# Kernel tuning notes

Measured on AMD Instinct MI355X. Metric: run time of the kernel, lower is better.

The kernel has to match this reference:

```python
import jax, jax.numpy as jnp
import numpy as np

SIGMA = 0.1
EPS = 1e-12

def setup_inputs() -> dict:
    key = jax.random.key(0)
    emb_org = jax.random.normal(key, (8192, 256), dtype=jnp.float32)
    return {"emb_org": emb_org}

def reference(emb_org):
    # L2-normalize rows (clamp norm at 1e-12 like torch)
    norm = jnp.clip(jnp.linalg.norm(emb_org, axis=1, keepdims=True), EPS, None)
    emb_n = emb_org / norm                      # [N, D]
    W = jnp.matmul(emb_n, emb_n.T) / SIGMA      # [N, N] cosine sim / sigma
    T = jax.nn.softmax(W, axis=1)               # row softmax
    emb_sft = jnp.matmul(T, emb_org)            # [N, D]
    return emb_sft
```

## Files before the change

kernel.cpp:

```cpp
#include <hip/hip_runtime.h>
#include <hip/hip_bf16.h>
#include <stdint.h>

#define NROWS 8192
#define DDIM  256
#define SIGMA_INV 10.0f

#define BM 64
#define BN 64
#define NSPLIT 4
#define JCHUNK (NROWS / NSPLIT)
#define NITER  (JCHUNK / BN)
#define PSTR   72
#define KCHB   1056

typedef __attribute__((ext_vector_type(8))) short bf16x8;
typedef __attribute__((ext_vector_type(4))) float f32x4;

__device__ inline unsigned short f2bf(float x) {
  __hip_bfloat16 h = __float2bfloat16(x);
  return *reinterpret_cast<unsigned short*>(&h);
}

__device__ inline void dma16(const void* g, void* l) {
  __builtin_amdgcn_global_load_lds(
      (const __attribute__((address_space(1))) unsigned int*)g,
      (__attribute__((address_space(3))) unsigned int*)l, 16, 0, 0);
}

__global__ __launch_bounds__(256) void normalize_k(const float* __restrict__ emb,
                                                   unsigned short* __restrict__ embn) {
  const int w = threadIdx.x >> 6, lane = threadIdx.x & 63;
  const int row = blockIdx.x * 4 + w;
  const float4* src = (const float4*)(emb + (size_t)row * DDIM);
  float4 v = src[lane];
  float ss = v.x * v.x + v.y * v.y + v.z * v.z + v.w * v.w;
  for (int off = 32; off >= 1; off >>= 1) ss += __shfl_xor(ss, off);
  const float sc = 1.0f / fmaxf(sqrtf(ss), 1e-12f);
  ushort4 o;
  o.x = f2bf(v.x * sc); o.y = f2bf(v.y * sc);
  o.z = f2bf(v.z * sc); o.w = f2bf(v.w * sc);
  ((ushort4*)(embn + (size_t)row * DDIM))[lane] = o;
}

__global__ __launch_bounds__(256) void transpose_k(const float* __restrict__ emb,
                                                   unsigned short* __restrict__ vt) {
  __shared__ float tile[64][65];
  const int r0 = blockIdx.x * 64, c0 = blockIdx.y * 64;
  const int tr = threadIdx.x >> 6, tc = threadIdx.x & 63;
  for (int i = 0; i < 16; ++i)
    tile[i * 4 + tr][tc] = emb[(size_t)(r0 + i * 4 + tr) * DDIM + c0 + tc];
  __syncthreads();
  for (int i = 0; i < 16; ++i)
    vt[(size_t)(c0 + i * 4 + tr) * NROWS + r0 + tc] = f2bf(tile[tc][i * 4 + tr]);
}

__global__ __launch_bounds__(256, 2) void fused_k(
    const unsigned short* __restrict__ embn,
    const unsigned short* __restrict__ vt,
    float* __restrict__ out,
    float* __restrict__ l_part)
{
  __shared__ char kn[32 * KCHB];
  __shared__ unsigned short pl[BM * PSTR];

  const int tid = threadIdx.x;
  const int w = tid >> 6, lane = tid & 63;
  const int mg = w >> 1, dh = w & 1;
  const int q = lane >> 4, c = lane & 15;
  const int chunk = blockIdx.x & 3;
  const int mblk = blockIdx.x >> 2;
  const int row0 = mblk * BM + mg * 32;
  const size_t j0base = (size_t)chunk * JCHUNK;

  bf16x8 qa[2][8];
  for (int mt = 0; mt < 2; ++mt)
    for (int k = 0; k < 8; ++k)
      qa[mt][k] = *(const bf16x8*)(embn + (size_t)(row0 + mt * 16 + c) * DDIM + k * 32 + q * 8);

  f32x4 oacc[2][8];
  for (int mt = 0; mt < 2; ++mt)
    for (int u = 0; u < 8; ++u) oacc[mt][u] = {0.f, 0.f, 0.f, 0.f};
  float lacc[2][4] = {};

  {
    const char* src = (const char*)(embn + j0base * DDIM);
    for (int cc = 0; cc < 8; ++cc) {
      const int ch = w * 8 + cc;
      dma16(src + ch * 1024 + lane * 16, kn + ch * KCHB + lane * 16);
    }
  }

  for (int it = 0; it < NITER; ++it) {
    const size_t j0 = j0base + (size_t)it * BN;
    __syncthreads();

    f32x4 sacc[2][2];
    for (int mt = 0; mt < 2; ++mt)
      for (int nt = 0; nt < 2; ++nt) sacc[mt][nt] = {0.f, 0.f, 0.f, 0.f};
    const int rb0 = (dh * 16 + (c >> 1)) * KCHB + (c & 1) * 512;
    const int rb1 = (dh * 16 + 8 + (c >> 1)) * KCHB + (c & 1) * 512;
    for (int k = 0; k < 8; ++k) {
      bf16x8 b0 = *(const bf16x8*)(kn + rb0 + k * 64 + q * 16);
      bf16x8 b1 = *(const bf16x8*)(kn + rb1 + k * 64 + q * 16);
      for (int mt = 0; mt < 2; ++mt) {
        sacc[mt][0] = __builtin_amdgcn_mfma_f32_16x16x32_bf16(qa[mt][k], b0, sacc[mt][0], 0, 0, 0);
        sacc[mt][1] = __builtin_amdgcn_mfma_f32_16x16x32_bf16(qa[mt][k], b1, sacc[mt][1], 0, 0, 0);
      }
    }

    bf16x8 vfrag[2][8];
    for (int kk = 0; kk < 2; ++kk)
      for (int u = 0; u < 8; ++u) {
        const int d = dh * 128 + u * 16 + c;
        vfrag[kk][u] = *(const bf16x8*)(vt + (size_t)d * NROWS + j0 + kk * 32 + q * 8);
      }

    for (int mt = 0; mt < 2; ++mt)
      for (int nt = 0; nt < 2; ++nt)
        for (int r = 0; r < 4; ++r) {
          const float p = __expf(fmaf(SIGMA_INV, sacc[mt][nt][r], -SIGMA_INV));
          lacc[mt][r] += p;
          pl[(mg * 32 + mt * 16 + q * 4 + r) * PSTR + dh * 32 + nt * 16 + c] = f2bf(p);
        }

    __syncthreads();

    for (int kk = 0; kk < 2; ++kk) {
      bf16x8 ap0 = *(const bf16x8*)(pl + (mg * 32 + c) * PSTR + kk * 32 + q * 8);
      bf16x8 ap1 = *(const bf16x8*)(pl + (mg * 32 + 16 + c) * PSTR + kk * 32 + q * 8);
      for (int u = 0; u < 8; ++u) {
        oacc[0][u] = __builtin_amdgcn_mfma_f32_16x16x32_bf16(ap0, vfrag[kk][u], oacc[0][u], 0, 0, 0);
        oacc[1][u] = __builtin_amdgcn_mfma_f32_16x16x32_bf16(ap1, vfrag[kk][u], oacc[1][u], 0, 0, 0);
      }
    }

    if (it + 1 < NITER) {
      const char* src = (const char*)(embn + (j0base + (size_t)(it + 1) * BN) * DDIM);
      for (int cc = 0; cc < 8; ++cc) {
        const int ch = w * 8 + cc;
        dma16(src + ch * 1024 + lane * 16, kn + ch * KCHB + lane * 16);
      }
    }
  }

  for (int mt = 0; mt < 2; ++mt)
    for (int r = 0; r < 4; ++r) {
      float s = lacc[mt][r];
      s += __shfl_xor(s, 1); s += __shfl_xor(s, 2);
      s += __shfl_xor(s, 4); s += __shfl_xor(s, 8);
      if (c == 0)
        atomicAdd(&l_part[row0 + mt * 16 + q * 4 + r], s);
    }
  for (int mt = 0; mt < 2; ++mt)
    for (int u = 0; u < 8; ++u)
      for (int r = 0; r < 4; ++r)
        atomicAdd(&out[(size_t)(row0 + mt * 16 + q * 4 + r) * DDIM + dh * 128 + u * 16 + c],
                  oacc[mt][u][r]);
}

__global__ __launch_bounds__(256) void finalize_k(float* __restrict__ out,
                                                  const float* __restrict__ l_part) {
  const int row = blockIdx.x, t = threadIdx.x;
  out[(size_t)row * DDIM + t] /= l_part[row];
}

extern "C" void kernel_launch(void* const* d_in, const int* in_sizes, int n_in,
                              void* d_out, int out_size, void* d_ws, size_t ws_size,
                              hipStream_t stream) {
  const float* emb = (const float*)d_in[0];
  float* out = (float*)d_out;
  char* ws = (char*)d_ws;
  unsigned short* embn = (unsigned short*)ws;
  unsigned short* vt   = (unsigned short*)(ws + ((size_t)4 << 20));
  float* l_part        = (float*)(ws + ((size_t)8 << 20));

  hipMemsetAsync(out, 0, (size_t)NROWS * DDIM * sizeof(float), stream);
  hipMemsetAsync(l_part, 0, (size_t)NROWS * sizeof(float), stream);

  normalize_k<<<NROWS / 4, 256, 0, stream>>>(emb, embn);
  transpose_k<<<dim3(NROWS / 64, DDIM / 64), 256, 0, stream>>>(emb, vt);
  fused_k<<<(NROWS / BM) * NSPLIT, 256, 0, stream>>>(embn, vt, out, l_part);
  finalize_k<<<NROWS, 256, 0, stream>>>(out, l_part);
}
```

Before: 237.5 us.

## Tile V layout, split keys six ways, prefetch K earlier with lighter barrier

Stores the transposed value matrix as contiguous per-64-row tiles, so each value fragment load touches one compact block instead of rows strided by the full sequence length. The key dimension is now split into six uneven chunks instead of four, and occupancy is raised to three blocks per SU. The next key tile's DMA is issued right after the P-store barrier, so it overlaps the PV MFMAs. That barrier waits only on LDS counters, not a full __syncthreads. Risks are register pressure under the higher launch bound and more atomic traffic from the extra splits.

New measurement: 398.3 us. 1.68x slower.

```diff
diff --git a/kernel.cpp b/kernel.cpp
--- a/kernel.cpp
+++ b/kernel.cpp
@@ -8,9 +8,8 @@
 
 #define BM 64
 #define BN 64
-#define NSPLIT 4
-#define JCHUNK (NROWS / NSPLIT)
-#define NITER  (JCHUNK / BN)
+#define NSPLIT 6
+#define NTILES (NROWS / BN)
 #define PSTR   72
 #define KCHB   1056
 
@@ -51,11 +50,12 @@
   for (int i = 0; i < 16; ++i)
     tile[i * 4 + tr][tc] = emb[(size_t)(r0 + i * 4 + tr) * DDIM + c0 + tc];
   __syncthreads();
+  unsigned short* dst = vt + (size_t)(r0 >> 6) * (DDIM * BN);
   for (int i = 0; i < 16; ++i)
-    vt[(size_t)(c0 + i * 4 + tr) * NROWS + r0 + tc] = f2bf(tile[tc][i * 4 + tr]);
+    dst[(size_t)(c0 + i * 4 + tr) * BN + tc] = f2bf(tile[tc][i * 4 + tr]);
 }
 
-__global__ __launch_bounds__(256, 2) void fused_k(
+__global__ __launch_bounds__(256, 3) void fused_k(
     const unsigned short* __restrict__ embn,
     const unsigned short* __restrict__ vt,
     float* __restrict__ out,
@@ -68,10 +68,11 @@
   const int w = tid >> 6, lane = tid & 63;
   const int mg = w >> 1, dh = w & 1;
   const int q = lane >> 4, c = lane & 15;
-  const int chunk = blockIdx.x & 3;
-  const int mblk = blockIdx.x >> 2;
+  const int chunk = blockIdx.x % NSPLIT;
+  const int mblk = blockIdx.x / NSPLIT;
   const int row0 = mblk * BM + mg * 32;
-  const size_t j0base = (size_t)chunk * JCHUNK;
+  const int t0 = (chunk * NTILES) / NSPLIT;
+  const int t1 = ((chunk + 1) * NTILES) / NSPLIT;
 
   bf16x8 qa[2][8];
   for (int mt = 0; mt < 2; ++mt)
@@ -84,15 +85,14 @@
   float lacc[2][4] = {};
 
   {
-    const char* src = (const char*)(embn + j0base * DDIM);
+    const char* src = (const char*)(embn + (size_t)t0 * BN * DDIM);
     for (int cc = 0; cc < 8; ++cc) {
       const int ch = w * 8 + cc;
       dma16(src + ch * 1024 + lane * 16, kn + ch * KCHB + lane * 16);
     }
   }
 
-  for (int it = 0; it < NITER; ++it) {
-    const size_t j0 = j0base + (size_t)it * BN;
+  for (int it = t0; it < t1; ++it) {
     __syncthreads();
 
     f32x4 sacc[2][2];
@@ -109,12 +109,11 @@
       }
     }
 
+    const unsigned short* vtile = vt + (size_t)it * (DDIM * BN);
     bf16x8 vfrag[2][8];
     for (int kk = 0; kk < 2; ++kk)
-      for (int u = 0; u < 8; ++u) {
-        const int d = dh * 128 + u * 16 + c;
-        vfrag[kk][u] = *(const bf16x8*)(vt + (size_t)d * NROWS + j0 + kk * 32 + q * 8);
-      }
+      for (int u = 0; u < 8; ++u)
+        vfrag[kk][u] = *(const bf16x8*)(vtile + (size_t)(dh * 128 + u * 16 + c) * BN + kk * 32 + q * 8);
 
     for (int mt = 0; mt < 2; ++mt)
       for (int nt = 0; nt < 2; ++nt)
@@ -124,7 +123,19 @@
           pl[(mg * 32 + mt * 16 + q * 4 + r) * PSTR + dh * 32 + nt * 16 + c] = f2bf(p);
         }
 
-    __syncthreads();
+    __builtin_amdgcn_sched_barrier(0);
+    asm volatile("s_waitcnt lgkmcnt(0)" ::: "memory");
+    __builtin_amdgcn_sched_barrier(0);
+    __builtin_amdgcn_s_barrier();
+    __builtin_amdgcn_sched_barrier(0);
+
+    if (it + 1 < t1) {
+      const char* src = (const char*)(embn + (size_t)(it + 1) * BN * DDIM);
+      for (int cc = 0; cc < 8; ++cc) {
+        const int ch = w * 8 + cc;
+        dma16(src + ch * 1024 + lane * 16, kn + ch * KCHB + lane * 16);
+      }
+    }
 
     for (int kk = 0; kk < 2; ++kk) {
       bf16x8 ap0 = *(const bf16x8*)(pl + (mg * 32 + c) * PSTR + kk * 32 + q * 8);
@@ -132,14 +143,6 @@
       for (int u = 0; u < 8; ++u) {
         oacc[0][u] = __builtin_amdgcn_mfma_f32_16x16x32_bf16(ap0, vfrag[kk][u], oacc[0][u], 0, 0, 0);
         oacc[1][u] = __builtin_amdgcn_mfma_f32_16x16x32_bf16(ap1, vfrag[kk][u], oacc[1][u], 0, 0, 0);
-      }
-    }
-
-    if (it + 1 < NITER) {
-      const char* src = (const char*)(embn + (j0base + (size_t)(it + 1) * BN) * DDIM);
-      for (int cc = 0; cc < 8; ++cc) {
-        const int ch = w * 8 + cc;
-        dma16(src + ch * 1024 + lane * 16, kn + ch * KCHB + lane * 16);
       }
     }
   }
```
